# Optimization experiments

Hardware: AMD Instinct MI355X
Metric: run time of the kernel (lower is better)

## Reference

```python
import jax, jax.numpy as jnp
from jax import lax
import numpy as np

H = 8  # hidden size


def setup_inputs() -> dict:
    key = jax.random.key(0)
    ks = jax.random.split(key, 7)
    B, T, I = 8192, 512, 1
    return {
        "x": jax.random.normal(ks[0], (B, T, I), dtype=jnp.float32),
        "W_ih": jax.random.normal(ks[1], (3 * H, I), dtype=jnp.float32) * 0.3,
        "W_hh": jax.random.normal(ks[2], (3 * H, H), dtype=jnp.float32) * 0.3,
        "b_ih": jax.random.normal(ks[3], (3 * H,), dtype=jnp.float32) * 0.1,
        "b_hh": jax.random.normal(ks[4], (3 * H,), dtype=jnp.float32) * 0.1,
        "W_fc": jax.random.normal(ks[5], (1, H), dtype=jnp.float32) * 0.3,
        "b_fc": jax.random.normal(ks[6], (1,), dtype=jnp.float32) * 0.1,
    }


def _gru_seq(x, W_ih, W_hh, b_ih, b_hh):
    # x: [B, T, I] -> output: [B, T, H]. PyTorch gate order: r, z, n.
    B = x.shape[0]
    # Precompute input-to-gate projections for all timesteps at once.
    xg = jnp.einsum("bti,gi->btg", x, W_ih) + b_ih  # [B, T, 3H]
    xg = jnp.moveaxis(xg, 1, 0)  # [T, B, 3H]

    def step(h, xt):
        hg = h @ W_hh.T + b_hh  # [B, 3H]
        xr, xz, xn = jnp.split(xt, 3, axis=-1)
        hr, hz, hn = jnp.split(hg, 3, axis=-1)
        r = jax.nn.sigmoid(xr + hr)
        z = jax.nn.sigmoid(xz + hz)
        n = jnp.tanh(xn + r * hn)
        h_new = (1.0 - z) * n + z * h
        return h_new, h_new

    h0 = jnp.zeros((B, H), dtype=x.dtype)
    _, hs = lax.scan(step, h0, xg)  # hs: [T, B, H]
    return jnp.moveaxis(hs, 0, 1)  # [B, T, H]


def reference(x, W_ih, W_hh, b_ih, b_hh, W_fc, b_fc):
    out = _gru_seq(x, W_ih, W_hh, b_ih, b_hh)  # [B, T, H]
    y_hat = out @ W_fc.T + b_fc  # [B, T, 1]
    return y_hat
```

## Files before the change

kernel.cpp:

```cpp
#include <hip/hip_runtime.h>

typedef __fp16 f16x2 __attribute__((ext_vector_type(2)));

#define T_LEN 512
#define LOG2E 1.44269504f

#define DPP_XOR1 0xB1
#define DPP_XOR2 0x4E
#define DPP_XOR3 0x1B
#define DPP_XOR8 0x128

#define DPPI(v, ctrl) __builtin_amdgcn_update_dpp(0, (v), (ctrl), 0xF, 0xF, true)
#define DPPF(v, ctrl) __int_as_float(DPPI(__float_as_int(v), (ctrl)))
#define DPPH2(v, ctrl) \
  __builtin_bit_cast(f16x2, DPPI(__builtin_bit_cast(int, (v)), (ctrl)))

#define FDOT2(a, b, c) __builtin_amdgcn_fdot2((a), (b), (c), false)

#define STEP(i, xi)                                                         \
  do {                                                                      \
          \
    const f16x2 p01 = __builtin_amdgcn_cvt_pkrtz(h, DPPF(h, DPP_XOR1));     \
    const f16x2 p45 = DPPH2(p01, DPP_XOR8);            \
    const f16x2 p23 = DPPH2(p01, DPP_XOR2);            \
    const f16x2 p67 = DPPH2(p45, DPP_XOR2);            \
                                       \
    float rA = FDOT2(p01, wr0, __builtin_fmaf(xi, wi_r, c_r));              \
    rA = FDOT2(p23, wr1, rA);                                               \
    float rB = FDOT2(p45, wr2, 0.0f);                                       \
    rB = FDOT2(p67, wr3, rB);                                               \
                                                                \
    float zA = FDOT2(p01, wz0, __builtin_fmaf(xi, wi_z, c_z));              \
    zA = FDOT2(p23, wz1, zA);                                               \
    float zB = FDOT2(p45, wz2, 0.0f);                                       \
    zB = FDOT2(p67, wz3, zB);                                               \
                                                     \
    float nA = FDOT2(p01, wn0, c_n);                                        \
    nA = FDOT2(p23, wn1, nA);                                               \
    float nB = FDOT2(p45, wn2, 0.0f);                                       \
    nB = FDOT2(p67, wn3, nB);                                               \
    const float r =                                                         \
        __builtin_amdgcn_rcpf(1.0f + __builtin_amdgcn_exp2f(rA + rB));      \
    const float z =                                                         \
        __builtin_amdgcn_rcpf(1.0f + __builtin_amdgcn_exp2f(zA + zB));      \
    const float omz = 1.0f - z;                  \
    const float zh = z * h;                      \
    const float xn = __builtin_fmaf(xi, wi_n, bi_n);                        \
    const float pn = __builtin_fmaf(r, nA + nB, xn);                        \
    const float uu =                                                        \
        __builtin_amdgcn_rcpf(1.0f + __builtin_amdgcn_exp2f(pn));           \
    const float nn = __builtin_fmaf(-2.0f, uu, 1.0f);             \
    h = __builtin_fmaf(omz, nn, zh);                \
                          \
    float m = __builtin_fmaf(h, wfc, bfc8);                                 \
    m += DPPF(m, DPP_XOR1);                                                 \
    m += DPPF(m, DPP_XOR2);                                                 \
    m += DPPF(m, DPP_XOR8);                                                 \
    ysel = is_##i ? m : ysel;                                               \
  } while (0)

__global__ void __launch_bounds__(256) gru_fused(
    const float* __restrict__ x, const float* __restrict__ W_ih,
    const float* __restrict__ W_hh, const float* __restrict__ b_ih,
    const float* __restrict__ b_hh, const float* __restrict__ W_fc,
    const float* __restrict__ b_fc, float* __restrict__ out) {
  const int tid = blockIdx.x * blockDim.x + threadIdx.x;
  const int pos = tid & 3;
  const int grp = (tid >> 2) & 1;
  const int hlf = (tid >> 3) & 1;
  const int j = pos | (hlf << 2);
  const int b = ((tid >> 4) << 1) | grp;

  const float* wr = W_hh + j * 8;
  const float* wz = W_hh + (8 + j) * 8;
  const float* wn = W_hh + (16 + j) * 8;
  const float SN = -LOG2E, SP = 2.0f * LOG2E;
  const f16x2 wr0 = __builtin_amdgcn_cvt_pkrtz(SN * wr[j ^ 0], SN * wr[j ^ 1]);
  const f16x2 wr1 = __builtin_amdgcn_cvt_pkrtz(SN * wr[j ^ 2], SN * wr[j ^ 3]);
  const f16x2 wr2 = __builtin_amdgcn_cvt_pkrtz(SN * wr[j ^ 4], SN * wr[j ^ 5]);
  const f16x2 wr3 = __builtin_amdgcn_cvt_pkrtz(SN * wr[j ^ 6], SN * wr[j ^ 7]);
  const f16x2 wz0 = __builtin_amdgcn_cvt_pkrtz(SN * wz[j ^ 0], SN * wz[j ^ 1]);
  const f16x2 wz1 = __builtin_amdgcn_cvt_pkrtz(SN * wz[j ^ 2], SN * wz[j ^ 3]);
  const f16x2 wz2 = __builtin_amdgcn_cvt_pkrtz(SN * wz[j ^ 4], SN * wz[j ^ 5]);
  const f16x2 wz3 = __builtin_amdgcn_cvt_pkrtz(SN * wz[j ^ 6], SN * wz[j ^ 7]);
  const f16x2 wn0 = __builtin_amdgcn_cvt_pkrtz(SP * wn[j ^ 0], SP * wn[j ^ 1]);
  const f16x2 wn1 = __builtin_amdgcn_cvt_pkrtz(SP * wn[j ^ 2], SP * wn[j ^ 3]);
  const f16x2 wn2 = __builtin_amdgcn_cvt_pkrtz(SP * wn[j ^ 4], SP * wn[j ^ 5]);
  const f16x2 wn3 = __builtin_amdgcn_cvt_pkrtz(SP * wn[j ^ 6], SP * wn[j ^ 7]);

  const float c_r = SN * (b_ih[j] + b_hh[j]);
  const float c_z = SN * (b_ih[8 + j] + b_hh[8 + j]);
  const float c_n = SP * b_hh[16 + j];
  const float bi_n = SP * b_ih[16 + j];
  const float wi_r = SN * W_ih[j], wi_z = SN * W_ih[8 + j],
              wi_n = SP * W_ih[16 + j];
  const float wfc = W_fc[j];
  const float bfc8 = b_fc[0] * 0.125f;

  const bool is_0 = (j == 0), is_1 = (j == 1), is_2 = (j == 2),
             is_3 = (j == 3);
  const bool is_4 = (j == 4), is_5 = (j == 5), is_6 = (j == 6),
             is_7 = (j == 7);

  const float* xp = x + (size_t)b * T_LEN;
  float* op = out + (size_t)b * T_LEN;

  float h = 0.0f;
  const float4* xq = reinterpret_cast<const float4*>(xp);
  float4 cA = xq[0], cB = xq[1];
  for (int t0 = 0; t0 < T_LEN; t0 += 8) {
    float4 nA4, nB4;
    if (t0 + 8 < T_LEN) {
      nA4 = xq[(t0 >> 2) + 2];
      nB4 = xq[(t0 >> 2) + 3];
    } else {
      nA4 = cA;
      nB4 = cB;
    }
    float ysel = 0.0f;
    STEP(0, cA.x);
    STEP(1, cA.y);
    STEP(2, cA.z);
    STEP(3, cA.w);
    STEP(4, cB.x);
    STEP(5, cB.y);
    STEP(6, cB.z);
    STEP(7, cB.w);
    op[t0 + j] = ysel;
    cA = nA4;
    cB = nB4;
  }
}

extern "C" void kernel_launch(void* const* d_in, const int* in_sizes, int n_in,
                              void* d_out, int out_size, void* d_ws,
                              size_t ws_size, hipStream_t stream) {
  const float* x = (const float*)d_in[0];
  const float* W_ih = (const float*)d_in[1];
  const float* W_hh = (const float*)d_in[2];
  const float* b_ih = (const float*)d_in[3];
  const float* b_hh = (const float*)d_in[4];
  const float* W_fc = (const float*)d_in[5];
  const float* b_fc = (const float*)d_in[6];
  float* out = (float*)d_out;

  const int B = in_sizes[0] / T_LEN;
  const int threads = B * 8;
  gru_fused<<<threads / 256, 256, 0, stream>>>(x, W_ih, W_hh, b_ih, b_hh, W_fc,
                                               b_fc, out);
}
```

Measured before the change: 59.84 us.

## Share sigmoid reciprocal, batch output reductions via butterfly, unroll 16 steps

The r and z sigmoids now share a single reciprocal of the product of their denominators, which takes one transcendental off the serial recurrence chain. The per-step 3-DPP allreduce for the FC output is replaced by a transpose-style butterfly over 8 steps (8+4+2 DPP adds with selects), so each lane ends with its own timestep's sum and DPP work moves off the critical h dependency. The time loop is unrolled to 16 steps with a larger x prefetch. Risks are higher register pressure and possible overflow when exp2 values are large and their product exceeds the float range.

After: 57.14 us. -4.5%, faster.

```diff
diff --git a/kernel.cpp b/kernel.cpp
--- a/kernel.cpp
+++ b/kernel.cpp
@@ -7,7 +7,6 @@
 
 #define DPP_XOR1 0xB1
 #define DPP_XOR2 0x4E
-#define DPP_XOR3 0x1B
 #define DPP_XOR8 0x128
 
 #define DPPI(v, ctrl) __builtin_amdgcn_update_dpp(0, (v), (ctrl), 0xF, 0xF, true)
@@ -17,46 +16,64 @@
 
 #define FDOT2(a, b, c) __builtin_amdgcn_fdot2((a), (b), (c), false)
 
-#define STEP(i, xi)                                                         \
+#define STEP(xi, mdst)                                                      \
   do {                                                                      \
-          \
     const f16x2 p01 = __builtin_amdgcn_cvt_pkrtz(h, DPPF(h, DPP_XOR1));     \
     const f16x2 p45 = DPPH2(p01, DPP_XOR8);            \
     const f16x2 p23 = DPPH2(p01, DPP_XOR2);            \
     const f16x2 p67 = DPPH2(p45, DPP_XOR2);            \
-                                       \
     float rA = FDOT2(p01, wr0, __builtin_fmaf(xi, wi_r, c_r));              \
     rA = FDOT2(p23, wr1, rA);                                               \
     float rB = FDOT2(p45, wr2, 0.0f);                                       \
     rB = FDOT2(p67, wr3, rB);                                               \
-                                                                \
     float zA = FDOT2(p01, wz0, __builtin_fmaf(xi, wi_z, c_z));              \
     zA = FDOT2(p23, wz1, zA);                                               \
     float zB = FDOT2(p45, wz2, 0.0f);                                       \
     zB = FDOT2(p67, wz3, zB);                                               \
-                                                     \
     float nA = FDOT2(p01, wn0, c_n);                                        \
     nA = FDOT2(p23, wn1, nA);                                               \
     float nB = FDOT2(p45, wn2, 0.0f);                                       \
     nB = FDOT2(p67, wn3, nB);                                               \
-    const float r =                                                         \
-        __builtin_amdgcn_rcpf(1.0f + __builtin_amdgcn_exp2f(rA + rB));      \
-    const float z =                                                         \
-        __builtin_amdgcn_rcpf(1.0f + __builtin_amdgcn_exp2f(zA + zB));      \
-    const float omz = 1.0f - z;                  \
-    const float zh = z * h;                      \
+    const float er = __builtin_amdgcn_exp2f(rA + rB);                       \
+    const float ez = __builtin_amdgcn_exp2f(zA + zB);                       \
+    const float dr = 1.0f + er, dz = 1.0f + ez;                             \
+    const float q = __builtin_amdgcn_rcpf(dr * dz);         \
+    const float r = dz * q;                       \
+    const float z = dr * q;                       \
+    const float omz = 1.0f - z;                                             \
+    const float zh = z * h;                                                 \
     const float xn = __builtin_fmaf(xi, wi_n, bi_n);                        \
     const float pn = __builtin_fmaf(r, nA + nB, xn);                        \
     const float uu =                                                        \
         __builtin_amdgcn_rcpf(1.0f + __builtin_amdgcn_exp2f(pn));           \
     const float nn = __builtin_fmaf(-2.0f, uu, 1.0f);             \
     h = __builtin_fmaf(omz, nn, zh);                \
-                          \
-    float m = __builtin_fmaf(h, wfc, bfc8);                                 \
-    m += DPPF(m, DPP_XOR1);                                                 \
-    m += DPPF(m, DPP_XOR2);                                                 \
-    m += DPPF(m, DPP_XOR8);                                                 \
-    ysel = is_##i ? m : ysel;                                               \
+    mdst = __builtin_fmaf(h, wfc, bfc8);                                    \
+  } while (0)
+
+#define BFLY_STORE(m0, m1, m2, m3, m4, m5, m6, m7, dst)                     \
+  do {                                                                      \
+    float s0 = m0 + DPPF(m0, DPP_XOR1);                                     \
+    float s1 = m1 + DPPF(m1, DPP_XOR1);                                     \
+    float s2 = m2 + DPPF(m2, DPP_XOR1);                                     \
+    float s3 = m3 + DPPF(m3, DPP_XOR1);                                     \
+    float s4 = m4 + DPPF(m4, DPP_XOR1);                                     \
+    float s5 = m5 + DPPF(m5, DPP_XOR1);                                     \
+    float s6 = m6 + DPPF(m6, DPP_XOR1);                                     \
+    float s7 = m7 + DPPF(m7, DPP_XOR1);                                     \
+    float t0_ = sel1 ? s1 : s0;                                             \
+    float t1_ = sel1 ? s3 : s2;                                             \
+    float t2_ = sel1 ? s5 : s4;                                             \
+    float t3_ = sel1 ? s7 : s6;                                             \
+    t0_ += DPPF(t0_, DPP_XOR2);                                             \
+    t1_ += DPPF(t1_, DPP_XOR2);                                             \
+    t2_ += DPPF(t2_, DPP_XOR2);                                             \
+    t3_ += DPPF(t3_, DPP_XOR2);                                             \
+    float u0_ = sel2 ? t1_ : t0_;                                           \
+    float u1_ = sel2 ? t3_ : t2_;                                           \
+    u0_ += DPPF(u0_, DPP_XOR8);                                             \
+    u1_ += DPPF(u1_, DPP_XOR8);                                             \
+    (dst) = sel4 ? u1_ : u0_;                                               \
   } while (0)
 
 __global__ void __launch_bounds__(256) gru_fused(
@@ -97,38 +114,48 @@
   const float wfc = W_fc[j];
   const float bfc8 = b_fc[0] * 0.125f;
 
-  const bool is_0 = (j == 0), is_1 = (j == 1), is_2 = (j == 2),
-             is_3 = (j == 3);
-  const bool is_4 = (j == 4), is_5 = (j == 5), is_6 = (j == 6),
-             is_7 = (j == 7);
+  const bool sel1 = (j & 1) != 0;
+  const bool sel2 = (j & 2) != 0;
+  const bool sel4 = (j & 4) != 0;
 
   const float* xp = x + (size_t)b * T_LEN;
   float* op = out + (size_t)b * T_LEN;
 
   float h = 0.0f;
   const float4* xq = reinterpret_cast<const float4*>(xp);
-  float4 cA = xq[0], cB = xq[1];
-  for (int t0 = 0; t0 < T_LEN; t0 += 8) {
-    float4 nA4, nB4;
-    if (t0 + 8 < T_LEN) {
-      nA4 = xq[(t0 >> 2) + 2];
-      nB4 = xq[(t0 >> 2) + 3];
-    } else {
-      nA4 = cA;
-      nB4 = cB;
+  float4 cA = xq[0], cB = xq[1], cC = xq[2], cD = xq[3];
+  for (int t0 = 0; t0 < T_LEN; t0 += 16) {
+    float4 nA4 = cA, nB4 = cB, nC4 = cC, nD4 = cD;
+    if (t0 + 16 < T_LEN) {
+      nA4 = xq[(t0 >> 2) + 4];
+      nB4 = xq[(t0 >> 2) + 5];
+      nC4 = xq[(t0 >> 2) + 6];
+      nD4 = xq[(t0 >> 2) + 7];
     }
-    float ysel = 0.0f;
-    STEP(0, cA.x);
-    STEP(1, cA.y);
-    STEP(2, cA.z);
-    STEP(3, cA.w);
-    STEP(4, cB.x);
-    STEP(5, cB.y);
-    STEP(6, cB.z);
-    STEP(7, cB.w);
-    op[t0 + j] = ysel;
+    float mA0, mA1, mA2, mA3, mA4, mA5, mA6, mA7;
+    float mB0, mB1, mB2, mB3, mB4, mB5, mB6, mB7;
+    STEP(cA.x, mA0);
+    STEP(cA.y, mA1);
+    STEP(cA.z, mA2);
+    STEP(cA.w, mA3);
+    STEP(cB.x, mA4);
+    STEP(cB.y, mA5);
+    STEP(cB.z, mA6);
+    STEP(cB.w, mA7);
+    BFLY_STORE(mA0, mA1, mA2, mA3, mA4, mA5, mA6, mA7, op[t0 + j]);
+    STEP(cC.x, mB0);
+    STEP(cC.y, mB1);
+    STEP(cC.z, mB2);
+    STEP(cC.w, mB3);
+    STEP(cD.x, mB4);
+    STEP(cD.y, mB5);
+    STEP(cD.z, mB6);
+    STEP(cD.w, mB7);
+    BFLY_STORE(mB0, mB1, mB2, mB3, mB4, mB5, mB6, mB7, op[t0 + 8 + j]);
     cA = nA4;
     cB = nB4;
+    cC = nC4;
+    cD = nD4;
   }
 }
 
```
